# Kernel tuning notes

Hardware: AMD Instinct MI355X
Metric: run time of the kernel (lower is better)

The kernel has to match this reference:

```python
import jax, jax.numpy as jnp
import numpy as np

STATE_DIM = 128
HIDDEN = 128
NUM_HEADS = 16
TEMPERATURE = 1.0
NEG_INF = float('-inf')


def setup_inputs() -> dict:
    key = jax.random.key(0)
    ks = jax.random.split(key, 8)
    B, S = 2, 512
    state_embeddings = jax.random.normal(ks[0], (B, S, STATE_DIM), dtype=jnp.float32)
    mask = jnp.ones((B, S, S), dtype=bool)
    # MLP params (Linear stores [in, out] here; we apply x @ W + b)
    W1 = jax.random.normal(ks[1], (2 * STATE_DIM, HIDDEN), dtype=jnp.float32) / np.sqrt(2 * STATE_DIM)
    b1 = jnp.zeros((HIDDEN,), dtype=jnp.float32)
    W2 = jax.random.normal(ks[2], (HIDDEN, HIDDEN), dtype=jnp.float32) / np.sqrt(HIDDEN)
    b2 = jnp.zeros((HIDDEN,), dtype=jnp.float32)
    W3 = jax.random.normal(ks[3], (HIDDEN, NUM_HEADS), dtype=jnp.float32) / np.sqrt(HIDDEN)
    b3 = jnp.zeros((NUM_HEADS,), dtype=jnp.float32)
    head_temperatures = jnp.ones((NUM_HEADS,), dtype=jnp.float32) * TEMPERATURE
    return {
        'state_embeddings': state_embeddings,
        'mask': mask,
        'W1': W1, 'b1': b1, 'W2': W2, 'b2': b2, 'W3': W3, 'b3': b3,
        'head_temperatures': head_temperatures,
    }


def reference(state_embeddings, mask, W1, b1, W2, b2, W3, b3, head_temperatures):
    # Split first Linear: cat([x_i, x_j]) @ W1 == x_i @ W1a + x_j @ W1b
    # This avoids materializing the [B, S, S, 2*state_dim] pairwise concat
    # while computing identical math.
    W1a, W1b = W1[:STATE_DIM], W1[STATE_DIM:]
    hi = jnp.einsum('bsd,dh->bsh', state_embeddings, W1a) + b1  # [B,S,H]
    hj = jnp.einsum('bsd,dh->bsh', state_embeddings, W1b)       # [B,S,H]
    h = jax.nn.relu(hi[:, :, None, :] + hj[:, None, :, :])       # [B,S,S,H]
    h = jax.nn.relu(jnp.einsum('bijh,hk->bijk', h, W2) + b2)     # [B,S,S,H]
    comp = jnp.einsum('bijh,hn->bijn', h, W3) + b3               # [B,S,S,heads]
    bias = jnp.transpose(comp, (0, 3, 1, 2))                     # [B,heads,S,S]
    bias = bias * head_temperatures[None, :, None, None]
    bias = jnp.where(mask[:, None, :, :], bias, NEG_INF)
    return bias
```

## Files before the change

### kernel.cpp

```cpp
#include <hip/hip_runtime.h>
#include <math.h>

typedef _Float16 half8 __attribute__((ext_vector_type(8)));
typedef _Float16 half4v __attribute__((ext_vector_type(4)));
typedef float floatx4 __attribute__((ext_vector_type(4)));

__global__ __launch_bounds__(256) void prep_kernel(
    const float* __restrict__ E,
    const float* __restrict__ W1,
    const float* __restrict__ b1,
    const float* __restrict__ W2,
    const float* __restrict__ W3,
    _Float16* __restrict__ hih,
    _Float16* __restrict__ hjh,
    _Float16* __restrict__ W2frag,
    _Float16* __restrict__ W3frag)
{
    const int blk = blockIdx.x;
    const int t = threadIdx.x;
    if (blk < 1024) {
        __shared__ float sE[128];
        if (t < 128) sE[t] = E[blk*128 + t];
        __syncthreads();
        const int half = t >> 7;
        const int k = t & 127;
        float acc = half ? 0.f : b1[k];
        const float* w1col = &W1[half*128*128 + k];
        #pragma unroll 8
        for (int d = 0; d < 128; ++d)
            acc = fmaf(sE[d], w1col[d*128], acc);
        if (half == 0) hih[blk*128 + k] = (_Float16)acc;
        else           hjh[blk*128 + k] = (_Float16)acc;
    } else if (blk == 1024) {
        for (int e = t; e < 16384; e += 256) {
            int q = e & 7, l = (e >> 3) & 63, g = e >> 9;
            int wr = g >> 4, nt = (g >> 2) & 3, ks = g & 3;
            int row = 64*wr + 16*nt + (l & 15);
            int k = ks*32 + (l >> 4)*8 + q;
            W2frag[e] = (_Float16)W2[k*128 + row];
        }
    } else {
        for (int e = t; e < 2048; e += 256) {
            int q = e & 7, l = (e >> 3) & 63, ks = e >> 9;
            int k = ks*32 + (l >> 4)*8 + q;
            W3frag[e] = (_Float16)W3[k*16 + (l & 15)];
        }
    }
}

__global__ __launch_bounds__(256, 3) void main_kernel(
    const _Float16* __restrict__ hih,
    const _Float16* __restrict__ hjh,
    const _Float16* __restrict__ W2frag,
    const _Float16* __restrict__ W3frag,
    const float* __restrict__ b2,
    const float* __restrict__ b3,
    const float* __restrict__ temps,
    const int* __restrict__ mask,
    float* __restrict__ out)
{
    constexpr int PADH = 136;
    __shared__ _Float16 sH[128 * PADH];

    const int tid = threadIdx.x;
    const int bid = blockIdx.x;
    const int b  = bid >> 11;
    const int i  = (bid >> 2) & 511;
    const int j0 = (bid & 3) << 7;

    const int lane = tid & 63;
    const int wave = tid >> 6;
    const int wr = wave >> 1;
    const int wc = wave & 1;
    const int lr = lane & 15;
    const int lq = lane >> 4;

    const half8 zero8 = {};
    const _Float16* hirow = &hih[(b*512 + i)*128];
    const _Float16* hjbase = &hjh[(b*512 + j0)*128];
    const half8* w2v = (const half8*)W2frag;

    half8 aW[4][4];
    #pragma unroll
    for (int nt = 0; nt < 4; ++nt)
        #pragma unroll
        for (int ks = 0; ks < 4; ++ks)
            aW[nt][ks] = w2v[((wr*4 + nt)*4 + ks)*64 + lane];

    half8 hiF[4];
    #pragma unroll
    for (int ks = 0; ks < 4; ++ks)
        hiF[ks] = *(const half8*)&hirow[ks*32 + lq*8];

    #pragma unroll
    for (int kk = 0; kk < 8; ++kk) {
        const int c = kk*256 + tid;
        const int row = c >> 4, col = c & 15;
        half8 v = *(const half8*)&hjbase[row*128 + col*8];
        *(half8*)&sH[row*PADH + col*8] = v;
    }
    __syncthreads();

    floatx4 acc[4][4] = {};
    #pragma unroll
    for (int ks = 0; ks < 4; ++ks) {
        const int kb = ks*32 + lq*8;
        half8 bF[4];
        #pragma unroll
        for (int mt = 0; mt < 4; ++mt) {
            const int m = 64*wc + 16*mt + lr;
            half8 hj8 = *(const half8*)&sH[m*PADH + kb];
            bF[mt] = __builtin_elementwise_max(hiF[ks] + hj8, zero8);
        }
        #pragma unroll
        for (int nt = 0; nt < 4; ++nt)
            #pragma unroll
            for (int mt = 0; mt < 4; ++mt)
                acc[nt][mt] = __builtin_amdgcn_mfma_f32_16x16x32_f16(
                    aW[nt][ks], bF[mt], acc[nt][mt], 0, 0, 0);
    }
    __syncthreads();

    #pragma unroll
    for (int nt = 0; nt < 4; ++nt) {
        const int nb = 64*wr + 16*nt + 4*lq;
        const float4 bv = *(const float4*)&b2[nb];
        #pragma unroll
        for (int mt = 0; mt < 4; ++mt) {
            const int m = 64*wc + 16*mt + lr;
            floatx4 v = acc[nt][mt];
            half4v o;
            o[0] = (_Float16)fmaxf(v[0] + bv.x, 0.f);
            o[1] = (_Float16)fmaxf(v[1] + bv.y, 0.f);
            o[2] = (_Float16)fmaxf(v[2] + bv.z, 0.f);
            o[3] = (_Float16)fmaxf(v[3] + bv.w, 0.f);
            *(half4v*)&sH[m*PADH + nb] = o;
        }
    }

    const int* mrow = &mask[(b*512 + i)*512];
    const int m0 = 32*wave;
    int4 mk0 = *(const int4*)&mrow[j0 + m0 + 4*lq];
    int4 mk1 = *(const int4*)&mrow[j0 + m0 + 16 + 4*lq];
    __syncthreads();

    const half8* w3v = (const half8*)W3frag;
    floatx4 acc2[2] = {};
    #pragma unroll
    for (int ks = 0; ks < 4; ++ks) {
        const int k0 = ks*32 + lq*8;
        half8 bW = w3v[ks*64 + lane];
        half8 a0 = *(const half8*)&sH[(m0 + lr)*PADH + k0];
        half8 a1 = *(const half8*)&sH[(m0 + 16 + lr)*PADH + k0];
        acc2[0] = __builtin_amdgcn_mfma_f32_16x16x32_f16(a0, bW, acc2[0], 0, 0, 0);
        acc2[1] = __builtin_amdgcn_mfma_f32_16x16x32_f16(a1, bW, acc2[1], 0, 0, 0);
    }

    const int n2 = lr;
    const float tempv = temps[n2];
    const float b3v = b3[n2];
    float* outp = &out[(((b*16 + n2)*512) + i)*512];
    {
        const int j = j0 + m0 + 4*lq;
        floatx4 v = acc2[0];
        float4 res;
        res.x = mk0.x ? (v[0] + b3v)*tempv : -INFINITY;
        res.y = mk0.y ? (v[1] + b3v)*tempv : -INFINITY;
        res.z = mk0.z ? (v[2] + b3v)*tempv : -INFINITY;
        res.w = mk0.w ? (v[3] + b3v)*tempv : -INFINITY;
        *(float4*)&outp[j] = res;
    }
    {
        const int j = j0 + m0 + 16 + 4*lq;
        floatx4 v = acc2[1];
        float4 res;
        res.x = mk1.x ? (v[0] + b3v)*tempv : -INFINITY;
        res.y = mk1.y ? (v[1] + b3v)*tempv : -INFINITY;
        res.z = mk1.z ? (v[2] + b3v)*tempv : -INFINITY;
        res.w = mk1.w ? (v[3] + b3v)*tempv : -INFINITY;
        *(float4*)&outp[j] = res;
    }
}

extern "C" void kernel_launch(void* const* d_in, const int* in_sizes, int n_in,
                              void* d_out, int out_size, void* d_ws, size_t ws_size,
                              hipStream_t stream)
{
    const float* E     = (const float*)d_in[0];
    const int* mask    = (const int*)d_in[1];
    const float* W1    = (const float*)d_in[2];
    const float* b1    = (const float*)d_in[3];
    const float* W2    = (const float*)d_in[4];
    const float* b2    = (const float*)d_in[5];
    const float* W3    = (const float*)d_in[6];
    const float* b3    = (const float*)d_in[7];
    const float* temps = (const float*)d_in[8];

    char* ws = (char*)d_ws;
    _Float16* hih = (_Float16*)ws;
    _Float16* hjh = (_Float16*)(ws + 262144);
    _Float16* W2f = (_Float16*)(ws + 524288);
    _Float16* W3f = W2f + 16384;

    prep_kernel<<<1026, 256, 0, stream>>>(E, W1, b1, W2, W3, hih, hjh, W2f, W3f);
    main_kernel<<<4096, 256, 0, stream>>>(hih, hjh, W2f, W3f, b2, b3, temps, mask,
                                          (float*)d_out);
}
```

Measured before the change: 115.4 us.

## Give each wave its own 32 rows to drop block barriers in main kernel

Each wave now owns a disjoint 32-row slice of the pairwise tile and computes all 128 hidden outputs for it. It loads its own hj rows into shared memory and reuses them for the second-layer output, so all three __syncthreads barriers go away. W2 fragments are streamed from global/L2 inside the k-loop instead of being held in registers, and the fp32-to-fp16 conversion uses packed cvt_pkrtz. In exchange the waves no longer share the W2 register tiles, so each wave reads the full W2 matrix, and the conversion changes from round-to-nearest to round-toward-zero.

Result: slower. 131.2 us (+13.6%).

```diff
diff --git a/kernel.cpp b/kernel.cpp
--- a/kernel.cpp
+++ b/kernel.cpp
@@ -3,6 +3,7 @@
 
 typedef _Float16 half8 __attribute__((ext_vector_type(8)));
 typedef _Float16 half4v __attribute__((ext_vector_type(4)));
+typedef __fp16 fp16x2 __attribute__((ext_vector_type(2)));
 typedef float floatx4 __attribute__((ext_vector_type(4)));
 
 __global__ __launch_bounds__(256) void prep_kernel(
@@ -34,8 +35,8 @@
     } else if (blk == 1024) {
         for (int e = t; e < 16384; e += 256) {
             int q = e & 7, l = (e >> 3) & 63, g = e >> 9;
-            int wr = g >> 4, nt = (g >> 2) & 3, ks = g & 3;
-            int row = 64*wr + 16*nt + (l & 15);
+            int NT = g >> 2, ks = g & 3;
+            int row = 16*NT + (l & 15);
             int k = ks*32 + (l >> 4)*8 + q;
             W2frag[e] = (_Float16)W2[k*128 + row];
         }
@@ -70,81 +71,72 @@
 
     const int lane = tid & 63;
     const int wave = tid >> 6;
-    const int wr = wave >> 1;
-    const int wc = wave & 1;
     const int lr = lane & 15;
     const int lq = lane >> 4;
+    const int m0 = 32*wave;
 
     const half8 zero8 = {};
     const _Float16* hirow = &hih[(b*512 + i)*128];
     const _Float16* hjbase = &hjh[(b*512 + j0)*128];
     const half8* w2v = (const half8*)W2frag;
-
-    half8 aW[4][4];
-    #pragma unroll
-    for (int nt = 0; nt < 4; ++nt)
-        #pragma unroll
-        for (int ks = 0; ks < 4; ++ks)
-            aW[nt][ks] = w2v[((wr*4 + nt)*4 + ks)*64 + lane];
+    const half8* w3v = (const half8*)W3frag;
 
     half8 hiF[4];
     #pragma unroll
     for (int ks = 0; ks < 4; ++ks)
         hiF[ks] = *(const half8*)&hirow[ks*32 + lq*8];
+    const int* mrow = &mask[(b*512 + i)*512];
+    const int4 mk0 = *(const int4*)&mrow[j0 + m0 + 4*lq];
+    const int4 mk1 = *(const int4*)&mrow[j0 + m0 + 16 + 4*lq];
 
     #pragma unroll
     for (int kk = 0; kk < 8; ++kk) {
-        const int c = kk*256 + tid;
-        const int row = c >> 4, col = c & 15;
-        half8 v = *(const half8*)&hjbase[row*128 + col*8];
-        *(half8*)&sH[row*PADH + col*8] = v;
-    }
-    __syncthreads();
-
-    floatx4 acc[4][4] = {};
+        const int c = kk*64 + lane;
+        const int row = m0 + (c >> 4), col = c & 15;
+        *(half8*)&sH[row*PADH + col*8] =
+            *(const half8*)&hjbase[row*128 + col*8];
+    }
+
+    floatx4 acc[8][2] = {};
     #pragma unroll
     for (int ks = 0; ks < 4; ++ks) {
         const int kb = ks*32 + lq*8;
-        half8 bF[4];
+        half8 bF[2];
         #pragma unroll
-        for (int mt = 0; mt < 4; ++mt) {
-            const int m = 64*wc + 16*mt + lr;
+        for (int mt = 0; mt < 2; ++mt) {
+            const int m = m0 + 16*mt + lr;
             half8 hj8 = *(const half8*)&sH[m*PADH + kb];
             bF[mt] = __builtin_elementwise_max(hiF[ks] + hj8, zero8);
         }
         #pragma unroll
-        for (int nt = 0; nt < 4; ++nt)
+        for (int nt = 0; nt < 8; ++nt) {
+            const half8 aW = w2v[(nt*4 + ks)*64 + lane];
             #pragma unroll
-            for (int mt = 0; mt < 4; ++mt)
+            for (int mt = 0; mt < 2; ++mt)
                 acc[nt][mt] = __builtin_amdgcn_mfma_f32_16x16x32_f16(
-                    aW[nt][ks], bF[mt], acc[nt][mt], 0, 0, 0);
-    }
-    __syncthreads();
-
-    #pragma unroll
-    for (int nt = 0; nt < 4; ++nt) {
-        const int nb = 64*wr + 16*nt + 4*lq;
+                    aW, bF[mt], acc[nt][mt], 0, 0, 0);
+        }
+    }
+
+    #pragma unroll
+    for (int nt = 0; nt < 8; ++nt) {
+        const int nb = 16*nt + 4*lq;
         const float4 bv = *(const float4*)&b2[nb];
         #pragma unroll
-        for (int mt = 0; mt < 4; ++mt) {
-            const int m = 64*wc + 16*mt + lr;
+        for (int mt = 0; mt < 2; ++mt) {
+            const int m = m0 + 16*mt + lr;
             floatx4 v = acc[nt][mt];
+            fp16x2 lo = __builtin_amdgcn_cvt_pkrtz(
+                fmaxf(v[0] + bv.x, 0.f), fmaxf(v[1] + bv.y, 0.f));
+            fp16x2 hi = __builtin_amdgcn_cvt_pkrtz(
+                fmaxf(v[2] + bv.z, 0.f), fmaxf(v[3] + bv.w, 0.f));
             half4v o;
-            o[0] = (_Float16)fmaxf(v[0] + bv.x, 0.f);
-            o[1] = (_Float16)fmaxf(v[1] + bv.y, 0.f);
-            o[2] = (_Float16)fmaxf(v[2] + bv.z, 0.f);
-            o[3] = (_Float16)fmaxf(v[3] + bv.w, 0.f);
+            o[0] = (_Float16)lo[0]; o[1] = (_Float16)lo[1];
+            o[2] = (_Float16)hi[0]; o[3] = (_Float16)hi[1];
             *(half4v*)&sH[m*PADH + nb] = o;
         }
     }
 
-    const int* mrow = &mask[(b*512 + i)*512];
-    const int m0 = 32*wave;
-    int4 mk0 = *(const int4*)&mrow[j0 + m0 + 4*lq];
-    int4 mk1 = *(const int4*)&mrow[j0 + m0 + 16 + 4*lq];
-    __syncthreads();
-
-    const half8* w3v = (const half8*)W3frag;
     floatx4 acc2[2] = {};
     #pragma unroll
     for (int ks = 0; ks < 4; ++ks) {
```
